# Optimization experiments

Hardware: AMD Instinct MI355X
Metric: run time of the kernel (lower is better)

Reference implementation:

```python
import jax, jax.numpy as jnp
import numpy as np

N_HEADS = 8
D_HEAD = 64  # n_embd=512 / n_heads=8


def setup_inputs() -> dict:
    key = jax.random.key(0)
    ks = jax.random.split(key, 5)
    B, T, C = 2, 4096, 512
    x = jax.random.normal(ks[0], (B, T, C), dtype=jnp.float32)
    s = 1.0 / np.sqrt(C)
    Wq = jax.random.normal(ks[1], (C, C), dtype=jnp.float32) * s
    Wk = jax.random.normal(ks[2], (C, C), dtype=jnp.float32) * s
    Wv = jax.random.normal(ks[3], (C, C), dtype=jnp.float32) * s
    Wout = jax.random.normal(ks[4], (C, C), dtype=jnp.float32) * s
    return {"x": x, "Wq": Wq, "Wk": Wk, "Wv": Wv, "Wout": Wout}


def reference(x, Wq, Wk, Wv, Wout):
    # x: [B,T,C]; nn.Linear(y) = y @ W.T, here weights stored as [C,C] used directly
    B, T, C = x.shape
    H, D = N_HEADS, D_HEAD
    q = (x @ Wq.T).reshape(B, T, H, D).transpose(0, 2, 1, 3)  # [B,H,T,D]
    k = (x @ Wk.T).reshape(B, T, H, D).transpose(0, 2, 1, 3)
    v = (x @ Wv.T).reshape(B, T, H, D).transpose(0, 2, 1, 3)
    att = jnp.einsum('bhqd,bhkd->bhqk', q, k) / jnp.sqrt(jnp.float32(D))  # [B,H,T,T]
    causal = jnp.tril(jnp.ones((T, T), dtype=bool))
    att = jnp.where(causal, att, -jnp.inf)
    att = jax.nn.softmax(att, axis=-1)
    # dropout is identity in eval mode (p=0)
    y = jnp.einsum('bhqk,bhkd->bhqd', att, v)  # [B,H,T,D]
    y = y.transpose(0, 2, 1, 3).reshape(B, T, C)
    return y @ Wout.T
```

## Files before the change

### kernel.cpp

```cpp
#include <hip/hip_runtime.h>
#include <hip/hip_bf16.h>
#include <math.h>
#include <stdint.h>

using bf16 = __hip_bfloat16;
typedef __attribute__((ext_vector_type(8))) short short8;
typedef __attribute__((ext_vector_type(4))) short short4v;
typedef __attribute__((ext_vector_type(4))) float float4v;

#define MFMA16(a, b, c) __builtin_amdgcn_mfma_f32_16x16x32_bf16(a, b, c, 0, 0, 0)

__device__ __forceinline__ short bfbits(float f) {
  bf16 h = (bf16)f;
  return *(short*)&h;
}

__device__ __forceinline__ short8 ld_cvt8(const float* p) {
  union { float4v v[2]; float f[8]; } u;
  u.v[0] = *(const float4v*)p;
  u.v[1] = *(const float4v*)(p + 4);
  short8 r;
#pragma unroll
  for (int j = 0; j < 8; j++) r[j] = bfbits(u.f[j]);
  return r;
}

__device__ __forceinline__ void gload16(const bf16* g, bf16* l) {
  __builtin_amdgcn_global_load_lds(
      (const __attribute__((address_space(1))) void*)g,
      (__attribute__((address_space(3))) void*)l, 16, 0, 0);
}

__global__ __launch_bounds__(256) void conv_all(
    const float* __restrict__ x, const float* __restrict__ w0,
    const float* __restrict__ w1, const float* __restrict__ w2,
    const float* __restrict__ w3, bf16* __restrict__ cx,
    bf16* __restrict__ cw) {
  size_t gid = ((size_t)blockIdx.x * 256 + threadIdx.x) * 8;
  const float* src;
  bf16* dst;
  size_t off;
  if (gid < 4194304) {
    src = x; dst = cx; off = gid;
  } else {
    size_t r = gid - 4194304;
    int wi = (int)(r >> 18);
    src = wi == 0 ? w0 : wi == 1 ? w1 : wi == 2 ? w2 : w3;
    dst = cw + ((size_t)wi << 18);
    off = r & 262143;
  }
  *(short8*)(dst + off) = ld_cvt8(src + off);
}

template <int MODE, int MT>
__device__ __forceinline__ void gemm_body(bf16* As, bf16* Bs,
                                          const bf16* __restrict__ A,
                                          const bf16* __restrict__ W,
                                          void* __restrict__ outp,
                                          float oscale) {
  constexpr int MI = MT / 32;
  const int bm = blockIdx.x * MT, bn = blockIdx.y * 128;
  const int tid = threadIdx.x;
  const int lane = tid & 63;
  const int wave = tid >> 6;
  const int lr = lane & 15, quad = lane >> 4;
  const int wm = (wave & 1) * (MT / 2), wn = (wave >> 1) * 64;

  const int srow = lane >> 3;
  const int scl = (lane & 7) ^ (srow & 7);
  const int rsw = lr & 7;

  float4v acc[MI][4] = {};

  for (int k0 = 0; k0 < 512; k0 += 64) {
    __syncthreads();
#pragma unroll
    for (int j = 0; j < MT / 32; j++) {
      const int m = wave + 4 * j;
      gload16(&A[(size_t)(bm + 8 * m + srow) * 512 + k0 + scl * 8],
              &As[(8 * m) * 64]);
    }
#pragma unroll
    for (int j = 0; j < 4; j++) {
      const int m = wave + 4 * j;
      gload16(&W[(size_t)(bn + 8 * m + srow) * 512 + k0 + scl * 8],
              &Bs[(8 * m) * 64]);
    }
    __syncthreads();
#pragma unroll
    for (int kk = 0; kk < 2; kk++) {
      short8 af[MI], bfv[4];
#pragma unroll
      for (int i = 0; i < MI; i++)
        af[i] = *(const short8*)
            &As[(wm + i * 16 + lr) * 64 + ((4 * kk + quad) ^ rsw) * 8];
#pragma unroll
      for (int i = 0; i < 4; i++)
        bfv[i] = *(const short8*)
            &Bs[(wn + i * 16 + lr) * 64 + ((4 * kk + quad) ^ rsw) * 8];
#pragma unroll
      for (int mi = 0; mi < MI; mi++)
#pragma unroll
        for (int ni = 0; ni < 4; ni++)
          acc[mi][ni] = MFMA16(af[mi], bfv[ni], acc[mi][ni]);
    }
  }

  const int row0 = bm + wm + quad * 4;
  const int col0 = bn + wn + lr;
#pragma unroll
  for (int mi = 0; mi < MI; mi++) {
#pragma unroll
    for (int ni = 0; ni < 4; ni++) {
      const int col = col0 + ni * 16;
      if (MODE == 1) {
        float* out = (float*)outp;
#pragma unroll
        for (int i = 0; i < 4; i++) {
          int m = row0 + mi * 16 + i;
          out[(size_t)m * 512 + col] = acc[mi][ni][i];
        }
      } else if (MODE == 0) {
        bf16* out = (bf16*)outp;
        const int hh = col >> 6, d = col & 63;
#pragma unroll
        for (int i = 0; i < 4; i++) {
          int m = row0 + mi * 16 + i;
          int bb = m >> 12, t = m & 4095;
          out[(((size_t)(bb * 8 + hh) * 4096 + t) << 6) + d] =
              (bf16)(acc[mi][ni][i] * oscale);
        }
      } else {
        bf16* out = (bf16*)outp;
        const int hh = col >> 6, d = col & 63;
        int m0 = row0 + mi * 16;
        int bb = m0 >> 12, t0 = m0 & 4095;
        short4v pk;
#pragma unroll
        for (int i = 0; i < 4; i++) pk[i] = bfbits(acc[mi][ni][i]);
        *(short4v*)&out[(((size_t)(bb * 8 + hh) * 64 + d) << 12) + t0] = pk;
      }
    }
  }
}

#define QSCALE 0.18033688f

__global__ __launch_bounds__(256) void qkv_kernel(
    const bf16* __restrict__ cx, const bf16* __restrict__ cW,
    bf16* q, bf16* k, bf16* vt) {
  __shared__ __align__(16) bf16 As[128 * 64];
  __shared__ __align__(16) bf16 Bs[128 * 64];
  if (blockIdx.z == 0)      gemm_body<0, 128>(As, Bs, cx, cW, q, QSCALE);
  else if (blockIdx.z == 1) gemm_body<0, 128>(As, Bs, cx, cW + 262144, k, 1.0f);
  else                      gemm_body<2, 128>(As, Bs, cx, cW + 2 * 262144, vt, 1.0f);
}

__global__ __launch_bounds__(256) void proj_kernel(
    const bf16* __restrict__ y, const bf16* __restrict__ cWout,
    float* __restrict__ out) {
  __shared__ __align__(16) bf16 As[64 * 64];
  __shared__ __align__(16) bf16 Bs[128 * 64];
  gemm_body<1, 64>(As, Bs, y, cWout, out, 1.0f);
}

__device__ __forceinline__ int lsw(int row, int col) {
  return (row << 6) + (col ^ ((row & 7) << 3));
}

template <bool DIAG>
__device__ __forceinline__ void attn_step(const bf16* __restrict__ Kc,
                                          const bf16* __restrict__ Vc,
                                          short8 qf0, short8 qf1,
                                          int wave, int lr, int quad,
                                          float& l_i, float4v* O) {
  float4v S[4] = {};
#pragma unroll
  for (int nc = 0; nc < 4; nc++) {
    short8 kf0 = *(const short8*)&Kc[lsw(nc * 16 + lr, quad * 8)];
    short8 kf1 = *(const short8*)&Kc[lsw(nc * 16 + lr, 32 + quad * 8)];
    S[nc] = MFMA16(kf0, qf0, S[nc]);
    S[nc] = MFMA16(kf1, qf1, S[nc]);
  }

  short8 pf0, pf1;
#pragma unroll
  for (int nc = 0; nc < 4; nc++) {
#pragma unroll
    for (int i = 0; i < 4; i++) {
      float pv = exp2f(S[nc][i]);
      if (DIAG) {
        int kl = nc * 16 + quad * 4 + i;
        pv = (kl > wave * 16 + lr) ? 0.f : pv;
      }
      l_i += pv;
      short bb = bfbits(pv);
      if (nc == 0)      pf0[i] = bb;
      else if (nc == 1) pf0[4 + i] = bb;
      else if (nc == 2) pf1[i] = bb;
      else              pf1[4 + i] = bb;
    }
  }

#pragma unroll
  for (int nc = 0; nc < 4; nc++) {
    const int row = nc * 16 + lr;
    short8 vfa = *(const short8*)&Vc[lsw(row, quad * 8)];
    short8 vfb = *(const short8*)&Vc[lsw(row, 32 + quad * 8)];
    O[nc] = MFMA16(pf0, vfa, O[nc]);
    O[nc] = MFMA16(pf1, vfb, O[nc]);
  }
}

__device__ __forceinline__ void vstore_perm(bf16* Vb, int row, int vA,
                                            short8 rv) {
  short4v lo = __builtin_shufflevector(rv, rv, 0, 1, 2, 3);
  short4v hi = __builtin_shufflevector(rv, rv, 4, 5, 6, 7);
  *(short4v*)&Vb[lsw(row, vA)] = lo;
  *(short4v*)&Vb[lsw(row, vA + 8)] = hi;
}

__global__ __launch_bounds__(256, 4) void attn_kernel(const bf16* __restrict__ Qg,
                                                      const bf16* __restrict__ Kg,
                                                      const bf16* __restrict__ Vtg,
                                                      bf16* __restrict__ Y) {
  constexpr int T = 4096;
  __shared__ __align__(16) bf16 Ks[2][64 * 64];
  __shared__ __align__(16) bf16 Vts[2][64 * 64];

  const int bx = blockIdx.x;
  const int g = bx >> 8, r = bx & 255;
  const int a = r >> 4, hb = r & 15;
  const int qt = (g == 0) ? a : (g == 1) ? 16 + a : (g == 2) ? 63 - a : 47 - a;
  const int h = hb >> 1, b = hb & 1;
  const size_t ho = ((size_t)(b * 8 + h)) * T * 64;
  const bf16* Qh = Qg + ho;
  const bf16* Kh = Kg + ho;
  const bf16* Vth = Vtg + ho;

  const int tid = threadIdx.x;
  const int wave = tid >> 6, lane = tid & 63;
  const int lr = lane & 15, quad = lane >> 4;

  const int sr = tid >> 3;
  const int s = tid & 7;
  const int sc = s * 8;
  const int vA = 32 * (s >> 2) + 16 * (s & 1) + 4 * ((s >> 1) & 1);
  const bf16* ksrc0 = Kh + (size_t)sr * 64 + sc;
  const bf16* ksrc1 = ksrc0 + 32 * 64;
  const bf16* vsrc0 = Vth + (size_t)sr * T + sc;
  const bf16* vsrc1 = vsrc0 + (size_t)32 * T;
  const int d0 = lsw(sr, sc);
  const int d1 = lsw(sr + 32, sc);

  short8 rk0 = *(const short8*)ksrc0;
  short8 rk1 = *(const short8*)ksrc1;
  short8 rv0 = *(const short8*)vsrc0;
  short8 rv1 = *(const short8*)vsrc1;

  short8 qf0, qf1;
  for (int ss = tid; ss < 512; ss += 256) {
    int rr = ss >> 3, c = (ss & 7) * 8;
    *(short8*)&Ks[1][lsw(rr, c)] =
        *(const short8*)&Qh[(size_t)(qt * 64 + rr) * 64 + c];
  }
  __syncthreads();
  qf0 = *(const short8*)&Ks[1][lsw(wave * 16 + lr, quad * 8)];
  qf1 = *(const short8*)&Ks[1][lsw(wave * 16 + lr, 32 + quad * 8)];
  *(short8*)&Ks[0][d0] = rk0;
  *(short8*)&Ks[0][d1] = rk1;
  vstore_perm(Vts[0], sr, vA, rv0);
  vstore_perm(Vts[0], sr + 32, vA, rv1);
  __syncthreads();

  float l_i = 0.f;
  float4v O[4] = {};

  for (int kt = 0; kt < qt; kt++) {
    const int cur = kt & 1, nxt = cur ^ 1;
    {
      const size_t ko = (size_t)(kt + 1) * 4096;
      const size_t vo = (size_t)(kt + 1) * 64;
      rk0 = *(const short8*)(ksrc0 + ko);
      rk1 = *(const short8*)(ksrc1 + ko);
      rv0 = *(const short8*)(vsrc0 + vo);
      rv1 = *(const short8*)(vsrc1 + vo);
    }

    attn_step<false>(Ks[cur], Vts[cur], qf0, qf1, wave, lr, quad, l_i, O);

    *(short8*)&Ks[nxt][d0] = rk0;
    *(short8*)&Ks[nxt][d1] = rk1;
    vstore_perm(Vts[nxt], sr, vA, rv0);
    vstore_perm(Vts[nxt], sr + 32, vA, rv1);
    __syncthreads();
  }
  attn_step<true>(Ks[qt & 1], Vts[qt & 1], qf0, qf1, wave, lr, quad, l_i, O);

  l_i += __shfl_xor(l_i, 16, 64);
  l_i += __shfl_xor(l_i, 32, 64);
  const float linv = 1.f / l_i;
  float lrow[4];
#pragma unroll
  for (int i = 0; i < 4; i++) lrow[i] = __shfl(linv, quad * 4 + i, 64);

  const size_t yb = ((size_t)b * T + qt * 64 + wave * 16 + quad * 4) * 512 + h * 64;
#pragma unroll
  for (int nc = 0; nc < 4; nc++)
#pragma unroll
    for (int i = 0; i < 4; i++)
      Y[yb + (size_t)i * 512 + nc * 16 + lr] = (bf16)(O[nc][i] * lrow[i]);
}

extern "C" void kernel_launch(void* const* d_in, const int* in_sizes, int n_in,
                              void* d_out, int out_size, void* d_ws, size_t ws_size,
                              hipStream_t stream) {
  (void)out_size; (void)ws_size;
  const int NX = 8192 * 512;
  int xi = 0;
  for (int i = 0; i < n_in; i++)
    if (in_sizes[i] == NX) { xi = i; break; }
  const float* x = (const float*)d_in[xi];
  const float* wsrc[4];
  int wn = 0;
  for (int i = 0; i < n_in && wn < 4; i++)
    if (i != xi) wsrc[wn++] = (const float*)d_in[i];

  bf16* ws = (bf16*)d_ws;
  const size_t HE = (size_t)NX;
  bf16* q  = ws;
  bf16* k  = q + HE;
  bf16* yx = k + HE;
  bf16* cw = yx + HE;
  bf16* vt = (bf16*)d_out;
  float* out = (float*)d_out;

  conv_all<<<2560, 256, 0, stream>>>(x, wsrc[0], wsrc[1], wsrc[2], wsrc[3],
                                     yx, cw);
  qkv_kernel<<<dim3(64, 4, 3), 256, 0, stream>>>(yx, cw, q, k, vt);
  attn_kernel<<<1024, 256, 0, stream>>>(q, k, vt, yx);
  proj_kernel<<<dim3(128, 4), 256, 0, stream>>>(yx, cw + 3 * 262144, out);
}
```

Before: 162.7 us.

## Split causal attention KV range across two wave groups per block and merge partials

Doubles the attention block to 512 threads and gives each half of the block its own share of the causal KV tiles, with separate double-buffered LDS. The two partial outputs and row sums are combined through shared memory at the end. Row sums are now computed with an MFMA against a ones vector rather than scalar adds, and blocks are scheduled longest-first. This shortens the serial KV loop per block to cut tail latency, at the cost of more LDS per block, a merge step, and idle iterations for the half with fewer tiles.

```diff
diff --git a/kernel.cpp b/kernel.cpp
--- a/kernel.cpp
+++ b/kernel.cpp
@@ -171,9 +171,9 @@
 template <bool DIAG>
 __device__ __forceinline__ void attn_step(const bf16* __restrict__ Kc,
                                           const bf16* __restrict__ Vc,
-                                          short8 qf0, short8 qf1,
+                                          short8 qf0, short8 qf1, short8 ones,
                                           int wave, int lr, int quad,
-                                          float& l_i, float4v* O) {
+                                          float4v& Lacc, float4v* O) {
   float4v S[4] = {};
 #pragma unroll
   for (int nc = 0; nc < 4; nc++) {
@@ -193,7 +193,6 @@
         int kl = nc * 16 + quad * 4 + i;
         pv = (kl > wave * 16 + lr) ? 0.f : pv;
       }
-      l_i += pv;
       short bb = bfbits(pv);
       if (nc == 0)      pf0[i] = bb;
       else if (nc == 1) pf0[4 + i] = bb;
@@ -201,6 +200,9 @@
       else              pf1[4 + i] = bb;
     }
   }
+
+  Lacc = MFMA16(pf0, ones, Lacc);
+  Lacc = MFMA16(pf1, ones, Lacc);
 
 #pragma unroll
   for (int nc = 0; nc < 4; nc++) {
@@ -220,18 +222,16 @@
   *(short4v*)&Vb[lsw(row, vA + 8)] = hi;
 }
 
-__global__ __launch_bounds__(256, 4) void attn_kernel(const bf16* __restrict__ Qg,
+__global__ __launch_bounds__(512, 4) void attn_kernel(const bf16* __restrict__ Qg,
                                                       const bf16* __restrict__ Kg,
                                                       const bf16* __restrict__ Vtg,
                                                       bf16* __restrict__ Y) {
   constexpr int T = 4096;
-  __shared__ __align__(16) bf16 Ks[2][64 * 64];
-  __shared__ __align__(16) bf16 Vts[2][64 * 64];
+  __shared__ __align__(16) bf16 KV[2][2][2][64 * 64];
 
   const int bx = blockIdx.x;
-  const int g = bx >> 8, r = bx & 255;
-  const int a = r >> 4, hb = r & 15;
-  const int qt = (g == 0) ? a : (g == 1) ? 16 + a : (g == 2) ? 63 - a : 47 - a;
+  const int qt = 63 - (bx >> 4);
+  const int hb = bx & 15;
   const int h = hb >> 1, b = hb & 1;
   const size_t ho = ((size_t)(b * 8 + h)) * T * 64;
   const bf16* Qh = Qg + ho;
@@ -239,13 +239,25 @@
   const bf16* Vth = Vtg + ho;
 
   const int tid = threadIdx.x;
-  const int wave = tid >> 6, lane = tid & 63;
+  const int G = tid >> 8;
+  const int t = tid & 255;
+  const int wave = t >> 6, lane = t & 63;
   const int lr = lane & 15, quad = lane >> 4;
 
-  const int sr = tid >> 3;
-  const int s = tid & 7;
-  const int sc = s * 8;
-  const int vA = 32 * (s >> 2) + 16 * (s & 1) + 4 * ((s >> 1) & 1);
+  const int S0 = (qt + 2) >> 1;
+  const int S1 = qt + 1 - S0;
+  const int kbase = G ? S0 : 0;
+  const int mysteps = G ? S1 : S0;
+
+  bf16* const Kb0 = KV[G][0][0];
+  bf16* const Kb1 = KV[G][1][0];
+  bf16* const Vb0 = KV[G][0][1];
+  bf16* const Vb1 = KV[G][1][1];
+
+  const int sr = t >> 3;
+  const int s8 = t & 7;
+  const int sc = s8 * 8;
+  const int vA = 32 * (s8 >> 2) + 16 * (s8 & 1) + 4 * ((s8 >> 1) & 1);
   const bf16* ksrc0 = Kh + (size_t)sr * 64 + sc;
   const bf16* ksrc1 = ksrc0 + 32 * 64;
   const bf16* vsrc0 = Vth + (size_t)sr * T + sc;
@@ -253,63 +265,101 @@
   const int d0 = lsw(sr, sc);
   const int d1 = lsw(sr + 32, sc);
 
-  short8 rk0 = *(const short8*)ksrc0;
-  short8 rk1 = *(const short8*)ksrc1;
-  short8 rv0 = *(const short8*)vsrc0;
-  short8 rv1 = *(const short8*)vsrc1;
-
-  short8 qf0, qf1;
-  for (int ss = tid; ss < 512; ss += 256) {
-    int rr = ss >> 3, c = (ss & 7) * 8;
-    *(short8*)&Ks[1][lsw(rr, c)] =
+  short8 rk0, rk1, rv0, rv1;
+  if (mysteps > 0) {
+    const size_t ko = (size_t)kbase * 4096;
+    const size_t vo = (size_t)kbase * 64;
+    rk0 = *(const short8*)(ksrc0 + ko);
+    rk1 = *(const short8*)(ksrc1 + ko);
+    rv0 = *(const short8*)(vsrc0 + vo);
+    rv1 = *(const short8*)(vsrc1 + vo);
+  }
+
+  {
+    int rr = tid >> 3, c = (tid & 7) * 8;
+    *(short8*)&KV[0][1][0][lsw(rr, c)] =
         *(const short8*)&Qh[(size_t)(qt * 64 + rr) * 64 + c];
   }
   __syncthreads();
-  qf0 = *(const short8*)&Ks[1][lsw(wave * 16 + lr, quad * 8)];
-  qf1 = *(const short8*)&Ks[1][lsw(wave * 16 + lr, 32 + quad * 8)];
-  *(short8*)&Ks[0][d0] = rk0;
-  *(short8*)&Ks[0][d1] = rk1;
-  vstore_perm(Vts[0], sr, vA, rv0);
-  vstore_perm(Vts[0], sr + 32, vA, rv1);
+  short8 qf0 = *(const short8*)&KV[0][1][0][lsw(wave * 16 + lr, quad * 8)];
+  short8 qf1 = *(const short8*)&KV[0][1][0][lsw(wave * 16 + lr, 32 + quad * 8)];
+  if (mysteps > 0) {
+    *(short8*)&Kb0[d0] = rk0;
+    *(short8*)&Kb0[d1] = rk1;
+    vstore_perm(Vb0, sr, vA, rv0);
+    vstore_perm(Vb0, sr + 32, vA, rv1);
+  }
   __syncthreads();
 
-  float l_i = 0.f;
+  short8 ones;
+#pragma unroll
+  for (int j = 0; j < 8; j++) ones[j] = (short)0x3F80;
+
   float4v O[4] = {};
-
-  for (int kt = 0; kt < qt; kt++) {
-    const int cur = kt & 1, nxt = cur ^ 1;
-    {
-      const size_t ko = (size_t)(kt + 1) * 4096;
-      const size_t vo = (size_t)(kt + 1) * 64;
+  float4v Lacc = {};
+
+  for (int s = 0; s < S0; s++) {
+    const bool act = s < mysteps;
+    const bool pf = s + 1 < mysteps;
+    if (pf) {
+      const size_t ko = (size_t)(kbase + s + 1) * 4096;
+      const size_t vo = (size_t)(kbase + s + 1) * 64;
       rk0 = *(const short8*)(ksrc0 + ko);
       rk1 = *(const short8*)(ksrc1 + ko);
       rv0 = *(const short8*)(vsrc0 + vo);
       rv1 = *(const short8*)(vsrc1 + vo);
     }
 
-    attn_step<false>(Ks[cur], Vts[cur], qf0, qf1, wave, lr, quad, l_i, O);
-
-    *(short8*)&Ks[nxt][d0] = rk0;
-    *(short8*)&Ks[nxt][d1] = rk1;
-    vstore_perm(Vts[nxt], sr, vA, rv0);
-    vstore_perm(Vts[nxt], sr + 32, vA, rv1);
+    if (act) {
+      const bf16* Kc = (s & 1) ? Kb1 : Kb0;
+      const bf16* Vc = (s & 1) ? Vb1 : Vb0;
+      const int kt = kbase + s;
+      if (kt == qt) attn_step<true>(Kc, Vc, qf0, qf1, ones, wave, lr, quad, Lacc, O);
+      else          attn_step<false>(Kc, Vc, qf0, qf1, ones, wave, lr, quad, Lacc, O);
+    }
+
+    if (pf) {
+      bf16* Kn = (s & 1) ? Kb0 : Kb1;
+      bf16* Vn = (s & 1) ? Vb0 : Vb1;
+      *(short8*)&Kn[d0] = rk0;
+      *(short8*)&Kn[d1] = rk1;
+      vstore_perm(Vn, sr, vA, rv0);
+      vstore_perm(Vn, sr + 32, vA, rv1);
+    }
     __syncthreads();
   }
-  attn_step<true>(Ks[qt & 1], Vts[qt & 1], qf0, qf1, wave, lr, quad, l_i, O);
-
-  l_i += __shfl_xor(l_i, 16, 64);
-  l_i += __shfl_xor(l_i, 32, 64);
-  const float linv = 1.f / l_i;
-  float lrow[4];
-#pragma unroll
-  for (int i = 0; i < 4; i++) lrow[i] = __shfl(linv, quad * 4 + i, 64);
-
-  const size_t yb = ((size_t)b * T + qt * 64 + wave * 16 + quad * 4) * 512 + h * 64;
-#pragma unroll
-  for (int nc = 0; nc < 4; nc++)
-#pragma unroll
-    for (int i = 0; i < 4; i++)
-      Y[yb + (size_t)i * 512 + nc * 16 + lr] = (bf16)(O[nc][i] * lrow[i]);
+
+  float* Op = (float*)&KV[1][0][0][0];
+  float* Lp = Op + 64 * 64;
+  const int r0 = wave * 16 + quad * 4;
+  if (G == 1 && S1 > 0) {
+#pragma unroll
+    for (int nc = 0; nc < 4; nc++)
+#pragma unroll
+      for (int i = 0; i < 4; i++)
+        Op[(r0 + i) * 64 + nc * 16 + lr] = O[nc][i];
+    if (lr == 0) {
+#pragma unroll
+      for (int i = 0; i < 4; i++) Lp[r0 + i] = Lacc[i];
+    }
+  }
+  __syncthreads();
+  if (G == 0) {
+    float inv[4];
+#pragma unroll
+    for (int i = 0; i < 4; i++) {
+      float lt = Lacc[i] + (S1 > 0 ? Lp[r0 + i] : 0.f);
+      inv[i] = 1.f / lt;
+    }
+    const size_t yb = ((size_t)b * T + qt * 64 + r0) * 512 + h * 64;
+#pragma unroll
+    for (int nc = 0; nc < 4; nc++)
+#pragma unroll
+      for (int i = 0; i < 4; i++) {
+        float o = O[nc][i] + (S1 > 0 ? Op[(r0 + i) * 64 + nc * 16 + lr] : 0.f);
+        Y[yb + (size_t)i * 512 + nc * 16 + lr] = (bf16)(o * inv[i]);
+      }
+  }
 }
 
 extern "C" void kernel_launch(void* const* d_in, const int* in_sizes, int n_in,
@@ -338,6 +388,6 @@
   conv_all<<<2560, 256, 0, stream>>>(x, wsrc[0], wsrc[1], wsrc[2], wsrc[3],
                                      yx, cw);
   qkv_kernel<<<dim3(64, 4, 3), 256, 0, stream>>>(yx, cw, q, k, vt);
-  attn_kernel<<<1024, 256, 0, stream>>>(q, k, vt, yx);
+  attn_kernel<<<1024, 512, 0, stream>>>(q, k, vt, yx);
   proj_kernel<<<dim3(128, 4), 256, 0, stream>>>(yx, cw + 3 * 262144, out);
 }
```

New measurement: 165.5 us. No clear change (+1.8%).
